# Optimization experiments

Measured on AMD Instinct MI355X. Metric: run time of the kernel, lower is better.

The kernel has to match this reference:

```python
import jax, jax.numpy as jnp
import numpy as np

D_MODEL = 1024
N_HEADS = 16
HEAD_DIM = D_MODEL // N_HEADS
B, S = 2, 2048


def setup_inputs() -> dict:
    key = jax.random.key(0)
    ks = jax.random.split(key, 12)
    std = 1.0 / np.sqrt(D_MODEL)
    mk = lambda k: (jax.random.normal(k, (D_MODEL, D_MODEL), jnp.float32) * std)
    return {
        "query": jax.random.normal(ks[0], (B, S, D_MODEL), jnp.float32),
        "key": jax.random.normal(ks[1], (B, S, D_MODEL), jnp.float32),
        "value": jax.random.normal(ks[2], (B, S, D_MODEL), jnp.float32),
        "Wq": mk(ks[3]), "bq": jnp.zeros((D_MODEL,), jnp.float32),
        "Wk": mk(ks[4]), "bk": jnp.zeros((D_MODEL,), jnp.float32),
        "Wv": mk(ks[5]), "bv": jnp.zeros((D_MODEL,), jnp.float32),
        "Wo": mk(ks[6]), "bo": jnp.zeros((D_MODEL,), jnp.float32),
    }


def reference(query, key, value, Wq, bq, Wk, bk, Wv, bv, Wo, bo):
    b, s, d = query.shape
    # Linear projections (torch Linear: x @ W.T + b)
    q = query @ Wq.T + bq
    k = key @ Wk.T + bk
    v = value @ Wv.T + bv
    # [B, H, S, Dh]
    split = lambda x: x.reshape(b, -1, N_HEADS, HEAD_DIM).transpose(0, 2, 1, 3)
    qh, kh, vh = split(q), split(k), split(v)
    scores = jnp.einsum("bhqd,bhkd->bhqk", qh, kh) / jnp.sqrt(
        jnp.asarray(HEAD_DIM, qh.dtype))
    attn = jax.nn.softmax(scores, axis=-1)
    out = jnp.einsum("bhqk,bhkd->bhqd", attn, vh)
    out = out.transpose(0, 2, 1, 3).reshape(b, -1, N_HEADS * HEAD_DIM)
    return out @ Wo.T + bo
```

## Files before the change

### kernel.cpp

```cpp
#include <hip/hip_runtime.h>
#include <hip/hip_bf16.h>


typedef short bf16x8 __attribute__((ext_vector_type(8)));
typedef short bf16x4 __attribute__((ext_vector_type(4)));
typedef float f32x4  __attribute__((ext_vector_type(4)));

constexpr size_t NE = (size_t)4096 * 1024;
constexpr size_t NW = (size_t)1024 * 1024;

#if __has_builtin(__builtin_amdgcn_exp2f)
#define EXP2(x) __builtin_amdgcn_exp2f(x)
#else
#define EXP2(x) exp2f(x)
#endif

__device__ __forceinline__ short f2bf(float f) {
  __hip_bfloat16 h = __float2bfloat16(f);
  return *reinterpret_cast<short*>(&h);
}

__device__ __forceinline__ void cp16(const short* g, short* l) {
  __builtin_amdgcn_global_load_lds(
      (const __attribute__((address_space(1))) void*)g,
      (__attribute__((address_space(3))) void*)l, 16, 0, 0);
}

__global__ __launch_bounds__(256) void cvt_kernel(
    const float* q, const float* k, const float* v,
    const float* Wq, const float* Wk, const float* Wv, const float* Wo,
    short* qb, short* kb, short* vb,
    short* Wqb, short* Wkb, short* Wvb, short* Wob) {
  const int y = blockIdx.y;
  const float* s; short* d;
  if (y < 12) {
    const int t = y >> 2;
    const size_t off = (size_t)(y & 3) << 20;
    s = (t == 0 ? q : (t == 1 ? k : v)) + off;
    d = (t == 0 ? qb : (t == 1 ? kb : vb)) + off;
  } else {
    s = (y == 12 ? Wq : (y == 13 ? Wk : (y == 14 ? Wv : Wo)));
    d = (y == 12 ? Wqb : (y == 13 ? Wkb : (y == 14 ? Wvb : Wob)));
  }
  size_t i = (size_t)blockIdx.x * 256 + threadIdx.x;
  float4 val = ((const float4*)s)[i];
  bf16x4 o;
  o[0] = f2bf(val.x); o[1] = f2bf(val.y); o[2] = f2bf(val.z); o[3] = f2bf(val.w);
  ((bf16x4*)d)[i] = o;
}

__global__ __launch_bounds__(256) void gemm_qkv(
    const short* __restrict__ A0, const short* __restrict__ A1, const short* __restrict__ A2,
    const short* __restrict__ W0, const short* __restrict__ W1, const short* __restrict__ W2,
    const float* __restrict__ b0, const float* __restrict__ b1, const float* __restrict__ b2,
    short* __restrict__ C0, short* __restrict__ C1, short* __restrict__ Cv) {
  __shared__ short As[2][128 * 32];
  __shared__ short Bs[2][128 * 32];
  const int which = blockIdx.y;
  const short* A    = which == 0 ? A0 : (which == 1 ? A1 : A2);
  const short* W    = which == 0 ? W0 : (which == 1 ? W1 : W2);
  const float* bias = which == 0 ? b0 : (which == 1 ? b1 : b2);
  const float scale = which == 0 ? 0.18033688011112042f : 1.0f;

  const int tid  = threadIdx.x;
  const int bm   = (int)blockIdx.x >> 3;
  const int bn   = (int)blockIdx.x & 7;
  const int lane = tid & 63, wid = tid >> 6;
  const int g = lane >> 4, l15 = lane & 15;
  const int wm = (wid >> 1) * 64, wn = (wid & 1) * 64;

  const short* Ag = A + (size_t)(bm * 128 + (tid >> 2)) * 1024 + (tid & 3) * 8;
  const short* Wg = W + (size_t)(bn * 128 + (tid >> 2)) * 1024 + (tid & 3) * 8;
  const int wofs = wid * 512;

  f32x4 acc[4][4];
#pragma unroll
  for (int i = 0; i < 4; ++i)
#pragma unroll
    for (int j = 0; j < 4; ++j) acc[i][j] = (f32x4){0.f, 0.f, 0.f, 0.f};

  cp16(Ag,             As[0] + wofs);
  cp16(Ag + 64 * 1024, As[0] + wofs + 2048);
  cp16(Wg,             Bs[0] + wofs);
  cp16(Wg + 64 * 1024, Bs[0] + wofs + 2048);

  for (int r = 0; r < 32; ++r) {
    const int cur = r & 1;
    __syncthreads();
    if (r < 31) {
      const int kk = (r + 1) * 32, nxt = cur ^ 1;
      cp16(Ag + kk,             As[nxt] + wofs);
      cp16(Ag + 64 * 1024 + kk, As[nxt] + wofs + 2048);
      cp16(Wg + kk,             Bs[nxt] + wofs);
      cp16(Wg + 64 * 1024 + kk, Bs[nxt] + wofs + 2048);
    }
    bf16x8 af[4], bf[4];
#pragma unroll
    for (int mt = 0; mt < 4; ++mt)
      af[mt] = *(const bf16x8*)&As[cur][(wm + mt * 16 + l15) * 32 + g * 8];
#pragma unroll
    for (int nt = 0; nt < 4; ++nt)
      bf[nt] = *(const bf16x8*)&Bs[cur][(wn + nt * 16 + l15) * 32 + g * 8];
#pragma unroll
    for (int mt = 0; mt < 4; ++mt)
#pragma unroll
      for (int nt = 0; nt < 4; ++nt)
        acc[mt][nt] = __builtin_amdgcn_mfma_f32_16x16x32_bf16(
            af[mt], bf[nt], acc[mt][nt], 0, 0, 0);
  }

  const int col0 = bn * 128 + wn;
  if (which < 2) {
    short* C = which == 0 ? C0 : C1;
#pragma unroll
    for (int nt = 0; nt < 4; ++nt) {
      const int col = col0 + nt * 16 + l15;
      const float bb = bias[col];
#pragma unroll
      for (int mt = 0; mt < 4; ++mt) {
        const int m0 = bm * 128 + wm + mt * 16 + g * 4;
#pragma unroll
        for (int r = 0; r < 4; ++r)
          C[(size_t)(m0 + r) * 1024 + col] = f2bf((acc[mt][nt][r] + bb) * scale);
      }
    }
  } else {
#pragma unroll
    for (int nt = 0; nt < 4; ++nt) {
      const int col = col0 + nt * 16 + l15;
      const int h = col >> 6, dh = col & 63;
      const float bb = bias[col];
#pragma unroll
      for (int mt = 0; mt < 4; ++mt) {
        const int m0 = bm * 128 + wm + mt * 16 + g * 4;
        const int bb_ = m0 >> 11, s0 = m0 & 2047;
        bf16x4 o;
#pragma unroll
        for (int r = 0; r < 4; ++r) o[r] = f2bf(acc[mt][nt][r] + bb);
        *(bf16x4*)&Cv[(((size_t)bb_ * 16 + h) * 64 + dh) * 2048 + s0] = o;
      }
    }
  }
}

__global__ __launch_bounds__(256) void gemm_out(
    const short* __restrict__ A, const short* __restrict__ W,
    const float* __restrict__ bias, float* __restrict__ C) {
  __shared__ short As[2][64 * 32];
  __shared__ short Bs[2][128 * 32];
  const int tid  = threadIdx.x;
  const int bm   = (int)blockIdx.x >> 3;
  const int bn   = (int)blockIdx.x & 7;
  const int lane = tid & 63, wid = tid >> 6;
  const int g = lane >> 4, l15 = lane & 15;
  const int wm = (wid >> 1) * 32, wn = (wid & 1) * 64;

  const short* Ag = A + (size_t)(bm * 64 + (tid >> 2)) * 1024 + (tid & 3) * 8;
  const short* Wg = W + (size_t)(bn * 128 + (tid >> 2)) * 1024 + (tid & 3) * 8;
  const int wofs = wid * 512;

  f32x4 acc[2][4];
#pragma unroll
  for (int i = 0; i < 2; ++i)
#pragma unroll
    for (int j = 0; j < 4; ++j) acc[i][j] = (f32x4){0.f, 0.f, 0.f, 0.f};

  cp16(Ag,             As[0] + wofs);
  cp16(Wg,             Bs[0] + wofs);
  cp16(Wg + 64 * 1024, Bs[0] + wofs + 2048);

  for (int r = 0; r < 32; ++r) {
    const int cur = r & 1;
    __syncthreads();
    if (r < 31) {
      const int kk = (r + 1) * 32, nxt = cur ^ 1;
      cp16(Ag + kk,             As[nxt] + wofs);
      cp16(Wg + kk,             Bs[nxt] + wofs);
      cp16(Wg + 64 * 1024 + kk, Bs[nxt] + wofs + 2048);
    }
    bf16x8 af[2], bf[4];
#pragma unroll
    for (int mt = 0; mt < 2; ++mt)
      af[mt] = *(const bf16x8*)&As[cur][(wm + mt * 16 + l15) * 32 + g * 8];
#pragma unroll
    for (int nt = 0; nt < 4; ++nt)
      bf[nt] = *(const bf16x8*)&Bs[cur][(wn + nt * 16 + l15) * 32 + g * 8];
#pragma unroll
    for (int mt = 0; mt < 2; ++mt)
#pragma unroll
      for (int nt = 0; nt < 4; ++nt)
        acc[mt][nt] = __builtin_amdgcn_mfma_f32_16x16x32_bf16(
            af[mt], bf[nt], acc[mt][nt], 0, 0, 0);
  }

  const int col0 = bn * 128 + wn;
#pragma unroll
  for (int nt = 0; nt < 4; ++nt) {
    const int col = col0 + nt * 16 + l15;
    const float bb = bias[col];
#pragma unroll
    for (int mt = 0; mt < 2; ++mt) {
      const int m0 = bm * 64 + wm + mt * 16 + g * 4;
#pragma unroll
      for (int r = 0; r < 4; ++r)
        C[(size_t)(m0 + r) * 1024 + col] = acc[mt][nt][r] + bb;
    }
  }
}

__global__ __launch_bounds__(256) void attn_kernel(
    const short* __restrict__ Q, const short* __restrict__ K,
    const short* __restrict__ Vg, short* __restrict__ O) {
  __shared__ short Kt[2][64][72];
  __shared__ short Vt[2][64][72];
  __shared__ short Pt[4][32][72];

  const int tid  = threadIdx.x;
  const int qt   = (int)blockIdx.x & 15;
  const int bh   = (int)blockIdx.x >> 4;
  const int b    = bh >> 4, h = bh & 15;
  const int lane = tid & 63, wid = tid >> 6;
  const int g = lane >> 4, l15 = lane & 15;

  const int q0 = qt * 128 + wid * 32;
  bf16x8 qf[2][2];
#pragma unroll
  for (int mt = 0; mt < 2; ++mt) {
    const size_t base = (size_t)(b * 2048 + q0 + mt * 16 + l15) * 1024 + h * 64;
    qf[mt][0] = *(const bf16x8*)(Q + base + g * 8);
    qf[mt][1] = *(const bf16x8*)(Q + base + 32 + g * 8);
  }

  f32x4 o_acc[2][4];
#pragma unroll
  for (int i = 0; i < 2; ++i)
#pragma unroll
    for (int j = 0; j < 4; ++j) o_acc[i][j] = (f32x4){0.f, 0.f, 0.f, 0.f};
  float l_i[2][4];
#pragma unroll
  for (int i = 0; i < 2; ++i)
#pragma unroll
    for (int r = 0; r < 4; ++r) l_i[i][r] = 0.f;

  const int srow = tid >> 2, sch = tid & 3;
  const short* Kbase = K + (size_t)(b * 2048) * 1024 + h * 64 + sch * 8;
  const short* Vbase = Vg + (size_t)((b * 16 + h) * 64 + srow) * 2048 + sch * 8;

  bf16x8 nk0, nk1, nv0, nv1;
  {
    const short* krow = Kbase + (size_t)srow * 1024;
    nk0 = *(const bf16x8*)(krow);
    nk1 = *(const bf16x8*)(krow + 32);
    nv0 = *(const bf16x8*)(Vbase);
    nv1 = *(const bf16x8*)(Vbase + 32);
  }

  for (int kt = 0; kt < 32; ++kt) {
    const int cur = kt & 1;
    *(bf16x8*)&Kt[cur][srow][sch * 8]      = nk0;
    *(bf16x8*)&Kt[cur][srow][sch * 8 + 32] = nk1;
    *(bf16x8*)&Vt[cur][srow][sch * 8]      = nv0;
    *(bf16x8*)&Vt[cur][srow][sch * 8 + 32] = nv1;
    __syncthreads();

    if (kt < 31) {
      const short* krow = Kbase + (size_t)((kt + 1) * 64 + srow) * 1024;
      nk0 = *(const bf16x8*)(krow);
      nk1 = *(const bf16x8*)(krow + 32);
      nv0 = *(const bf16x8*)(Vbase + (kt + 1) * 64);
      nv1 = *(const bf16x8*)(Vbase + (kt + 1) * 64 + 32);
    }

    f32x4 sv[2][4];
#pragma unroll
    for (int nt = 0; nt < 4; ++nt) {
      bf16x8 kf0 = *(const bf16x8*)&Kt[cur][nt * 16 + l15][g * 8];
      bf16x8 kf1 = *(const bf16x8*)&Kt[cur][nt * 16 + l15][32 + g * 8];
#pragma unroll
      for (int mt = 0; mt < 2; ++mt) {
        f32x4 z = (f32x4){0.f, 0.f, 0.f, 0.f};
        z = __builtin_amdgcn_mfma_f32_16x16x32_bf16(qf[mt][0], kf0, z, 0, 0, 0);
        z = __builtin_amdgcn_mfma_f32_16x16x32_bf16(qf[mt][1], kf1, z, 0, 0, 0);
        sv[mt][nt] = z;
      }
    }

#pragma unroll
    for (int mt = 0; mt < 2; ++mt)
#pragma unroll
      for (int r = 0; r < 4; ++r) {
        float p0 = EXP2(sv[mt][0][r]);
        float p1 = EXP2(sv[mt][1][r]);
        float p2 = EXP2(sv[mt][2][r]);
        float p3 = EXP2(sv[mt][3][r]);
        l_i[mt][r] += (p0 + p1) + (p2 + p3);
        const int pr = mt * 16 + g * 4 + r;
        Pt[wid][pr][l15]      = f2bf(p0);
        Pt[wid][pr][16 + l15] = f2bf(p1);
        Pt[wid][pr][32 + l15] = f2bf(p2);
        Pt[wid][pr][48 + l15] = f2bf(p3);
      }

    bf16x8 pf[2][2];
#pragma unroll
    for (int mt = 0; mt < 2; ++mt) {
      pf[mt][0] = *(const bf16x8*)&Pt[wid][mt * 16 + l15][g * 8];
      pf[mt][1] = *(const bf16x8*)&Pt[wid][mt * 16 + l15][32 + g * 8];
    }
#pragma unroll
    for (int nt = 0; nt < 4; ++nt) {
      bf16x8 vf0 = *(const bf16x8*)&Vt[cur][nt * 16 + l15][g * 8];
      bf16x8 vf1 = *(const bf16x8*)&Vt[cur][nt * 16 + l15][32 + g * 8];
#pragma unroll
      for (int mt = 0; mt < 2; ++mt) {
        o_acc[mt][nt] = __builtin_amdgcn_mfma_f32_16x16x32_bf16(
            pf[mt][0], vf0, o_acc[mt][nt], 0, 0, 0);
        o_acc[mt][nt] = __builtin_amdgcn_mfma_f32_16x16x32_bf16(
            pf[mt][1], vf1, o_acc[mt][nt], 0, 0, 0);
      }
    }
  }

#pragma unroll
  for (int mt = 0; mt < 2; ++mt)
#pragma unroll
    for (int r = 0; r < 4; ++r) {
      float l = l_i[mt][r];
#pragma unroll
      for (int off = 1; off < 16; off <<= 1) l += __shfl_xor(l, off, 64);
      const float inv = 1.0f / l;
      const int row = q0 + mt * 16 + g * 4 + r;
      const size_t base = (size_t)(b * 2048 + row) * 1024 + h * 64;
#pragma unroll
      for (int nt = 0; nt < 4; ++nt)
        O[base + nt * 16 + l15] = f2bf(o_acc[mt][nt][r] * inv);
    }
}

extern "C" void kernel_launch(void* const* d_in, const int* in_sizes, int n_in,
                              void* d_out, int out_size, void* d_ws, size_t ws_size,
                              hipStream_t stream) {
  (void)in_sizes; (void)n_in; (void)out_size; (void)ws_size;
  const float* q  = (const float*)d_in[0];
  const float* k  = (const float*)d_in[1];
  const float* v  = (const float*)d_in[2];
  const float* Wq = (const float*)d_in[3];
  const float* bq = (const float*)d_in[4];
  const float* Wk = (const float*)d_in[5];
  const float* bk = (const float*)d_in[6];
  const float* Wv = (const float*)d_in[7];
  const float* bv = (const float*)d_in[8];
  const float* Wo = (const float*)d_in[9];
  const float* bo = (const float*)d_in[10];
  float* out = (float*)d_out;

  short* qb  = (short*)d_ws;
  short* kb  = qb + NE;
  short* vb  = kb + NE;
  short* Wqb = vb + NE;
  short* Wkb = Wqb + NW;
  short* Wvb = Wkb + NW;
  short* Wob = Wvb + NW;
  short* Qw  = Wob + NW;
  short* Kw  = Qw + NE;
  short* Vtg = Kw + NE;
  short* Ob  = qb;

  cvt_kernel<<<dim3(1024, 16), 256, 0, stream>>>(q, k, v, Wq, Wk, Wv, Wo,
                                                 qb, kb, vb, Wqb, Wkb, Wvb, Wob);
  gemm_qkv<<<dim3(256, 3), 256, 0, stream>>>(qb, kb, vb, Wqb, Wkb, Wvb,
                                             bq, bk, bv, Qw, Kw, Vtg);
  attn_kernel<<<512, 256, 0, stream>>>(Qw, Kw, Vtg, Ob);
  gemm_out<<<512, 256, 0, stream>>>(Ob, Wob, bo, out);
}
```

Before: 248.1 us.

## Double per-wave query rows in attention to reuse K/V tiles across more rows

Each attention wave now handles 64 query rows instead of 32, so a block covers 256 queries and the grid halves to 256 blocks. Each K/V tile loaded into shared memory is reused across twice as many rows, which halves K/V global traffic and the LDS fragment reads per MFMA. The cost is more registers per thread for accumulators and query fragments, a larger P scratch buffer, and only 256 blocks, which may not fill all compute units on a 256-CU part. Launch bounds now request one block per CU.

```diff
diff --git a/kernel.cpp b/kernel.cpp
--- a/kernel.cpp
+++ b/kernel.cpp
@@ -208,37 +208,37 @@
   }
 }
 
-__global__ __launch_bounds__(256) void attn_kernel(
+__global__ __launch_bounds__(256, 1) void attn_kernel(
     const short* __restrict__ Q, const short* __restrict__ K,
     const short* __restrict__ Vg, short* __restrict__ O) {
   __shared__ short Kt[2][64][72];
   __shared__ short Vt[2][64][72];
-  __shared__ short Pt[4][32][72];
+  __shared__ short Pt[4][64][72];
 
   const int tid  = threadIdx.x;
-  const int qt   = (int)blockIdx.x & 15;
-  const int bh   = (int)blockIdx.x >> 4;
+  const int qt   = (int)blockIdx.x & 7;
+  const int bh   = (int)blockIdx.x >> 3;
   const int b    = bh >> 4, h = bh & 15;
   const int lane = tid & 63, wid = tid >> 6;
   const int g = lane >> 4, l15 = lane & 15;
 
-  const int q0 = qt * 128 + wid * 32;
-  bf16x8 qf[2][2];
-#pragma unroll
-  for (int mt = 0; mt < 2; ++mt) {
+  const int q0 = qt * 256 + wid * 64;
+  bf16x8 qf[4][2];
+#pragma unroll
+  for (int mt = 0; mt < 4; ++mt) {
     const size_t base = (size_t)(b * 2048 + q0 + mt * 16 + l15) * 1024 + h * 64;
     qf[mt][0] = *(const bf16x8*)(Q + base + g * 8);
     qf[mt][1] = *(const bf16x8*)(Q + base + 32 + g * 8);
   }
 
-  f32x4 o_acc[2][4];
-#pragma unroll
-  for (int i = 0; i < 2; ++i)
+  f32x4 o_acc[4][4];
+#pragma unroll
+  for (int i = 0; i < 4; ++i)
 #pragma unroll
     for (int j = 0; j < 4; ++j) o_acc[i][j] = (f32x4){0.f, 0.f, 0.f, 0.f};
-  float l_i[2][4];
-#pragma unroll
-  for (int i = 0; i < 2; ++i)
+  float l_i[4][4];
+#pragma unroll
+  for (int i = 0; i < 4; ++i)
 #pragma unroll
     for (int r = 0; r < 4; ++r) l_i[i][r] = 0.f;
 
@@ -271,28 +271,29 @@
       nv1 = *(const bf16x8*)(Vbase + (kt + 1) * 64 + 32);
     }
 
-    f32x4 sv[2][4];
+    bf16x8 kf[4][2];
 #pragma unroll
     for (int nt = 0; nt < 4; ++nt) {
-      bf16x8 kf0 = *(const bf16x8*)&Kt[cur][nt * 16 + l15][g * 8];
-      bf16x8 kf1 = *(const bf16x8*)&Kt[cur][nt * 16 + l15][32 + g * 8];
-#pragma unroll
-      for (int mt = 0; mt < 2; ++mt) {
+      kf[nt][0] = *(const bf16x8*)&Kt[cur][nt * 16 + l15][g * 8];
+      kf[nt][1] = *(const bf16x8*)&Kt[cur][nt * 16 + l15][32 + g * 8];
+    }
+
+#pragma unroll
+    for (int mt = 0; mt < 4; ++mt) {
+      f32x4 sv[4];
+#pragma unroll
+      for (int nt = 0; nt < 4; ++nt) {
         f32x4 z = (f32x4){0.f, 0.f, 0.f, 0.f};
-        z = __builtin_amdgcn_mfma_f32_16x16x32_bf16(qf[mt][0], kf0, z, 0, 0, 0);
-        z = __builtin_amdgcn_mfma_f32_16x16x32_bf16(qf[mt][1], kf1, z, 0, 0, 0);
-        sv[mt][nt] = z;
-      }
-    }
-
-#pragma unroll
-    for (int mt = 0; mt < 2; ++mt)
+        z = __builtin_amdgcn_mfma_f32_16x16x32_bf16(qf[mt][0], kf[nt][0], z, 0, 0, 0);
+        z = __builtin_amdgcn_mfma_f32_16x16x32_bf16(qf[mt][1], kf[nt][1], z, 0, 0, 0);
+        sv[nt] = z;
+      }
 #pragma unroll
       for (int r = 0; r < 4; ++r) {
-        float p0 = EXP2(sv[mt][0][r]);
-        float p1 = EXP2(sv[mt][1][r]);
-        float p2 = EXP2(sv[mt][2][r]);
-        float p3 = EXP2(sv[mt][3][r]);
+        float p0 = EXP2(sv[0][r]);
+        float p1 = EXP2(sv[1][r]);
+        float p2 = EXP2(sv[2][r]);
+        float p3 = EXP2(sv[3][r]);
         l_i[mt][r] += (p0 + p1) + (p2 + p3);
         const int pr = mt * 16 + g * 4 + r;
         Pt[wid][pr][l15]      = f2bf(p0);
@@ -300,29 +301,30 @@
         Pt[wid][pr][32 + l15] = f2bf(p2);
         Pt[wid][pr][48 + l15] = f2bf(p3);
       }
-
-    bf16x8 pf[2][2];
-#pragma unroll
-    for (int mt = 0; mt < 2; ++mt) {
-      pf[mt][0] = *(const bf16x8*)&Pt[wid][mt * 16 + l15][g * 8];
-      pf[mt][1] = *(const bf16x8*)&Pt[wid][mt * 16 + l15][32 + g * 8];
-    }
+    }
+
+    bf16x8 vf[4][2];
 #pragma unroll
     for (int nt = 0; nt < 4; ++nt) {
-      bf16x8 vf0 = *(const bf16x8*)&Vt[cur][nt * 16 + l15][g * 8];
-      bf16x8 vf1 = *(const bf16x8*)&Vt[cur][nt * 16 + l15][32 + g * 8];
-#pragma unroll
-      for (int mt = 0; mt < 2; ++mt) {
+      vf[nt][0] = *(const bf16x8*)&Vt[cur][nt * 16 + l15][g * 8];
+      vf[nt][1] = *(const bf16x8*)&Vt[cur][nt * 16 + l15][32 + g * 8];
+    }
+#pragma unroll
+    for (int mt = 0; mt < 4; ++mt) {
+      bf16x8 pf0 = *(const bf16x8*)&Pt[wid][mt * 16 + l15][g * 8];
+      bf16x8 pf1 = *(const bf16x8*)&Pt[wid][mt * 16 + l15][32 + g * 8];
+#pragma unroll
+      for (int nt = 0; nt < 4; ++nt) {
         o_acc[mt][nt] = __builtin_amdgcn_mfma_f32_16x16x32_bf16(
-            pf[mt][0], vf0, o_acc[mt][nt], 0, 0, 0);
+            pf0, vf[nt][0], o_acc[mt][nt], 0, 0, 0);
         o_acc[mt][nt] = __builtin_amdgcn_mfma_f32_16x16x32_bf16(
-            pf[mt][1], vf1, o_acc[mt][nt], 0, 0, 0);
-      }
-    }
-  }
-
-#pragma unroll
-  for (int mt = 0; mt < 2; ++mt)
+            pf1, vf[nt][1], o_acc[mt][nt], 0, 0, 0);
+      }
+    }
+  }
+
+#pragma unroll
+  for (int mt = 0; mt < 4; ++mt)
 #pragma unroll
     for (int r = 0; r < 4; ++r) {
       float l = l_i[mt][r];
@@ -370,6 +372,6 @@
                                                  qb, kb, vb, Wqb, Wkb, Wvb, Wob);
   gemm_qkv<<<dim3(256, 3), 256, 0, stream>>>(qb, kb, vb, Wqb, Wkb, Wvb,
                                              bq, bk, bv, Qw, Kw, Vtg);
-  attn_kernel<<<512, 256, 0, stream>>>(Qw, Kw, Vtg, Ob);
+  attn_kernel<<<256, 256, 0, stream>>>(Qw, Kw, Vtg, Ob);
   gemm_out<<<512, 256, 0, stream>>>(Ob, Wob, bo, out);
 }
```

Result: no change. 245.1 us (-1.2%).
